# Kernel tuning notes

Measured on AMD Instinct MI355X. Metric: run time of the kernel, lower is better.

Reference implementation:

```python
import jax, jax.numpy as jnp
import numpy as np

DIM = 1024
HEADS = 16
HEAD_DIM = DIM // HEADS
SCALE = HEAD_DIM ** -0.5


def setup_inputs() -> dict:
    key = jax.random.key(0)
    k1, k2, k3 = jax.random.split(key, 3)
    x = jax.random.normal(k1, (4, 2048, DIM), dtype=jnp.float32)
    # nn.Linear weight shape [out, in]; y = x @ W.T
    W_qkv = jax.random.normal(k2, (3 * DIM, DIM), dtype=jnp.float32) * (DIM ** -0.5)
    W_proj = jax.random.normal(k3, (DIM, DIM), dtype=jnp.float32) * (DIM ** -0.5)
    b_proj = jnp.zeros((DIM,), dtype=jnp.float32)
    return {"x": x, "W_qkv": W_qkv, "W_proj": W_proj, "b_proj": b_proj}


def reference(x, W_qkv, W_proj, b_proj):
    B, N, C = x.shape
    qkv = x @ W_qkv.T  # [B, N, 3C]
    qkv = qkv.reshape(B, N, 3, HEADS, HEAD_DIM).transpose(2, 0, 3, 1, 4)  # [3,B,H,N,D]
    q, k, v = qkv[0], qkv[1], qkv[2]
    attn = jnp.einsum('bhnd,bhmd->bhnm', q, k) * SCALE
    attn = jax.nn.softmax(attn, axis=-1)
    out = jnp.einsum('bhnm,bhmd->bhnd', attn, v)  # [B,H,N,D]
    out = out.transpose(0, 2, 1, 3).reshape(B, N, C)
    return out @ W_proj.T + b_proj
```

## Files before the change

kernel.cpp:

```cpp
#include <hip/hip_runtime.h>
#include <hip/hip_bf16.h>
#include <stdint.h>

typedef __attribute__((ext_vector_type(8))) __bf16 bf16x8;
typedef __attribute__((ext_vector_type(4))) float f32x4;
typedef __attribute__((ext_vector_type(16))) float f32x16;
typedef __attribute__((ext_vector_type(8))) unsigned short u16x8;
typedef __attribute__((ext_vector_type(4))) unsigned int u32x4;

#define DIM 1024
#define SEQ 2048
#define BATCH 4
#define MROWS (BATCH*SEQ)
#define QK_SCALE 0.1803368801111204f

__device__ __forceinline__ unsigned short f2bf(float f) {
  unsigned int u = __float_as_uint(f);
  u += 0x7fff + ((u >> 16) & 1);
  return (unsigned short)(u >> 16);
}

__device__ __forceinline__ void async16(const void* g, void* l) {
  __builtin_amdgcn_global_load_lds(
      (const __attribute__((address_space(1))) unsigned int*)g,
      (__attribute__((address_space(3))) unsigned int*)l, 16, 0, 0);
}

__device__ __forceinline__ unsigned cvtpk(float lo, float hi) {
  unsigned r;
  asm("v_cvt_pk_bf16_f32 %0, %1, %2" : "=v"(r) : "v"(lo), "v"(hi));
  return r;
}

__global__ __launch_bounds__(256) void cvt3(
    const float* __restrict__ x, const float* __restrict__ w1,
    const float* __restrict__ w2, unsigned short* __restrict__ xb,
    unsigned short* __restrict__ w1b, unsigned short* __restrict__ w2b) {
  const size_t NX = (size_t)MROWS * DIM;
  const size_t NW1 = (size_t)3 * DIM * DIM;
  const size_t NW2 = (size_t)DIM * DIM;
  size_t i = ((size_t)blockIdx.x * blockDim.x + threadIdx.x) * 8;
  const float* s; unsigned short* d; size_t off;
  if (i < NX) { s = x; d = xb; off = i; }
  else if (i < NX + NW1) { s = w1; d = w1b; off = i - NX; }
  else if (i < NX + NW1 + NW2) { s = w2; d = w2b; off = i - NX - NW1; }
  else return;
  float4 a = *(const float4*)(s + off);
  float4 b = *(const float4*)(s + off + 4);
  u16x8 r;
  r[0] = f2bf(a.x); r[1] = f2bf(a.y); r[2] = f2bf(a.z); r[3] = f2bf(a.w);
  r[4] = f2bf(b.x); r[5] = f2bf(b.y); r[6] = f2bf(b.z); r[7] = f2bf(b.w);
  *(u16x8*)(d + off) = r;
}

template<int OUT_BF16>
__global__ __launch_bounds__(256) void gemm_bt(
    const unsigned short* __restrict__ A, const unsigned short* __restrict__ Bt,
    unsigned short* __restrict__ Cb, float* __restrict__ Cf,
    const float* __restrict__ bias, int M, int N, int K,
    float qscale, int qcols)
{
  __shared__ unsigned short Asm[128 * 64];
  __shared__ unsigned short Bsm[128 * 64];

  int nwg = gridDim.x;
  int bid = blockIdx.x;
  int cpx = nwg >> 3;
  int wg = (bid & 7) * cpx + (bid >> 3);
  int ntn = N >> 7;
  int tn = wg % ntn, tm = wg / ntn;

  int t = threadIdx.x, l = t & 63, w = t >> 6;
  int lr = l & 15, lg = l >> 4;
  int wr = w >> 1, wc = w & 1;

  f32x4 acc[4][4] = {};

  const unsigned short* Ab = A + (size_t)tm * 128 * K;
  const unsigned short* Bb = Bt + (size_t)tn * 128 * K;

  for (int k0 = 0; k0 < K; k0 += 64) {
    #pragma unroll
    for (int i = 0; i < 4; ++i) {
      int idx = i * 256 + t;
      int row = idx >> 3, cc = (idx & 7) * 8;
      async16(Ab + (size_t)row * K + k0 + cc, (char*)Asm + idx * 16);
      async16(Bb + (size_t)row * K + k0 + cc, (char*)Bsm + idx * 16);
    }
    __syncthreads();
    #pragma unroll
    for (int kk = 0; kk < 2; ++kk) {
      bf16x8 af[4], bfr[4];
      #pragma unroll
      for (int m = 0; m < 4; ++m)
        af[m] = *(const bf16x8*)&Asm[(wr * 64 + m * 16 + lr) * 64 + kk * 32 + lg * 8];
      #pragma unroll
      for (int n = 0; n < 4; ++n)
        bfr[n] = *(const bf16x8*)&Bsm[(wc * 64 + n * 16 + lr) * 64 + kk * 32 + lg * 8];
      #pragma unroll
      for (int m = 0; m < 4; ++m)
        #pragma unroll
        for (int n = 0; n < 4; ++n)
          acc[m][n] = __builtin_amdgcn_mfma_f32_16x16x32_bf16(af[m], bfr[n], acc[m][n], 0, 0, 0);
    }
    __syncthreads();
  }

  #pragma unroll
  for (int m = 0; m < 4; ++m)
    #pragma unroll
    for (int n = 0; n < 4; ++n) {
      int col = tn * 128 + wc * 64 + n * 16 + lr;
      float cs = (OUT_BF16 && col < qcols) ? qscale : 1.0f;
      #pragma unroll
      for (int j = 0; j < 4; ++j) {
        int row = tm * 128 + wr * 64 + m * 16 + lg * 4 + j;
        if (OUT_BF16) Cb[(size_t)row * N + col] = f2bf(acc[m][n][j] * cs);
        else          Cf[(size_t)row * N + col] = acc[m][n][j] + bias[col];
      }
    }
}

__global__ __launch_bounds__(256, 4) void attn_fwd(
    const unsigned short* __restrict__ qkv, unsigned short* __restrict__ out)
{
  __shared__ unsigned short Ksm[2][64 * 64];
  __shared__ unsigned short Vt[2][64 * 64];
  __shared__ float bcast[4][32];

  const int sb = (blockIdx.x & 7) * 128 + (blockIdx.x >> 3);
  const int bh = sb >> 4;
  const int qt = sb & 15;
  const int b = bh >> 4, h = bh & 15;
  const int t = threadIdx.x, wid = t >> 6, l = t & 63;
  const int ql = l & 31, hi = l >> 5;

  const size_t RS = 3 * DIM;
  const unsigned short* base = qkv + (size_t)b * SEQ * RS + h * 64;
  const unsigned short* kb = base + DIM;
  const unsigned short* vp = base + 2 * DIM;

  const int qrow = qt * 128 + wid * 32 + ql;
  bf16x8 qf[4];
  #pragma unroll
  for (int s = 0; s < 4; ++s)
    qf[s] = *(const bf16x8*)(base + (size_t)qrow * RS + s * 16 + hi * 8);

  f32x16 oacc[2] = {};
  float rlp = 0.f;

  #define STAGE_K(KT, BUF)                                                   \
    _Pragma("unroll")                                                        \
    for (int i_ = 0; i_ < 2; ++i_) {                                         \
      int idx_ = i_ * 256 + t;                                               \
      int row_ = idx_ >> 3, pc_ = idx_ & 7;                                  \
      async16(kb + (size_t)((KT) * 64 + row_) * RS + (pc_ ^ (row_ & 7)) * 8, \
              (char*)(BUF) + idx_ * 16);                                     \
    }

  #define LOAD_V(KT, VA, VB)                                                 \
    {                                                                        \
      const unsigned short* p_ = vp + (size_t)((KT) * 64 + (t & 63)) * RS +  \
                                 (t >> 6) * 16;                              \
      VA = *(const u16x8*)p_;                                                \
      VB = *(const u16x8*)(p_ + 8);                                          \
    }

  #define WRITE_V(BUF, VA, VB)                                               \
    {                                                                        \
      int vn_ = t & 63, dg_ = t >> 6;                                        \
      int pc_ = (vn_ & 51) | ((vn_ & 4) << 1) | ((vn_ & 8) >> 1);            \
      _Pragma("unroll")                                                      \
      for (int j_ = 0; j_ < 8; ++j_) {                                       \
        int d0_ = dg_ * 16 + j_, d1_ = d0_ + 8;                              \
        (BUF)[d0_ * 64 + (((pc_ >> 3) ^ (d0_ & 7)) << 3) + (pc_ & 7)] = (VA)[j_]; \
        (BUF)[d1_ * 64 + (((pc_ >> 3) ^ (d1_ & 7)) << 3) + (pc_ & 7)] = (VB)[j_]; \
      }                                                                      \
    }

  {
    u16x8 va, vb2;
    STAGE_K(0, Ksm[0]);
    LOAD_V(0, va, vb2);
    WRITE_V(Vt[0], va, vb2);
  }
  __syncthreads();

  const int NT = SEQ / 64;
  int cur = 0;
  for (int kt = 0; kt < NT; ++kt) {
    u16x8 va, vb2;
    const bool pf = (kt + 1 < NT);
    if (pf) {
      STAGE_K(kt + 1, Ksm[cur ^ 1]);
      LOAD_V(kt + 1, va, vb2);
    }

    f32x16 st[2];
    __builtin_amdgcn_s_setprio(1);
    #pragma unroll
    for (int ti = 0; ti < 2; ++ti) {
      f32x16 a = {};
      int row = ti * 32 + ql;
      #pragma unroll
      for (int s = 0; s < 4; ++s) {
        bf16x8 af = *(const bf16x8*)&Ksm[cur][row * 64 + (((2 * s + hi) ^ (row & 7)) << 3)];
        a = __builtin_amdgcn_mfma_f32_32x32x16_bf16(af, qf[s], a, 0, 0, 0);
      }
      st[ti] = a;
    }
    __builtin_amdgcn_s_setprio(0);

    #pragma unroll
    for (int ti = 0; ti < 2; ++ti)
      #pragma unroll
      for (int r = 0; r < 16; ++r)
        st[ti][r] = __builtin_exp2f(st[ti][r]);
    float s0[8];
    #pragma unroll
    for (int r = 0; r < 8; ++r)
      s0[r] = (st[0][r] + st[0][r + 8]) + (st[1][r] + st[1][r + 8]);
    rlp += ((s0[0] + s0[1]) + (s0[2] + s0[3])) + ((s0[4] + s0[5]) + (s0[6] + s0[7]));

    bf16x8 pa[4];
    #pragma unroll
    for (int ti = 0; ti < 2; ++ti) {
      union { u32x4 u; bf16x8 v; } c0, c1;
      #pragma unroll
      for (int j = 0; j < 4; ++j) {
        c0.u[j] = cvtpk(st[ti][2 * j],     st[ti][2 * j + 1]);
        c1.u[j] = cvtpk(st[ti][8 + 2 * j], st[ti][8 + 2 * j + 1]);
      }
      pa[2 * ti]     = c0.v;
      pa[2 * ti + 1] = c1.v;
    }

    __builtin_amdgcn_s_setprio(1);
    #pragma unroll
    for (int c = 0; c < 4; ++c) {
      #pragma unroll
      for (int dh = 0; dh < 2; ++dh) {
        int row = dh * 32 + ql;
        bf16x8 vf = *(const bf16x8*)&Vt[cur][row * 64 + (((2 * c + hi) ^ (row & 7)) << 3)];
        oacc[dh] = __builtin_amdgcn_mfma_f32_32x32x16_bf16(pa[c], vf, oacc[dh], 0, 0, 0);
      }
    }
    __builtin_amdgcn_s_setprio(0);

    if (pf) { WRITE_V(Vt[cur ^ 1], va, vb2); }
    __syncthreads();
    cur ^= 1;
  }

  {
    float rl = rlp + __shfl_xor(rlp, 32);
    float inv = 1.0f / rl;
    if (l < 32) bcast[wid][l] = inv;
    asm volatile("s_waitcnt lgkmcnt(0)" ::: "memory");
    __builtin_amdgcn_sched_barrier(0);
    f32x4 ig[4];
    #pragma unroll
    for (int g = 0; g < 4; ++g)
      ig[g] = *(const f32x4*)&bcast[wid][8 * g + 4 * hi];
    #pragma unroll
    for (int dh = 0; dh < 2; ++dh) {
      #pragma unroll
      for (int g = 0; g < 4; ++g) {
        #pragma unroll
        for (int r2 = 0; r2 < 4; ++r2) {
          int q = r2 + 8 * g + 4 * hi;
          int grow = b * SEQ + qt * 128 + wid * 32 + q;
          int gcol = h * 64 + dh * 32 + ql;
          out[(size_t)grow * DIM + gcol] = f2bf(oacc[dh][g * 4 + r2] * ig[g][r2]);
        }
      }
    }
  }
  #undef STAGE_K
  #undef LOAD_V
  #undef WRITE_V
}

extern "C" void kernel_launch(void* const* d_in, const int* in_sizes, int n_in,
                              void* d_out, int out_size, void* d_ws, size_t ws_size,
                              hipStream_t stream) {
  const float* x     = (const float*)d_in[0];
  const float* Wqkv  = (const float*)d_in[1];
  const float* Wproj = (const float*)d_in[2];
  const float* bproj = (const float*)d_in[3];
  float* out = (float*)d_out;

  unsigned short* xb    = (unsigned short*)d_ws;
  unsigned short* w1b   = xb + (size_t)MROWS * DIM;
  unsigned short* w2b   = w1b + (size_t)3 * DIM * DIM;
  unsigned short* qkvb  = w2b + (size_t)DIM * DIM;
  unsigned short* attnb = qkvb + (size_t)MROWS * 3 * DIM;

  cvt3<<<6144, 256, 0, stream>>>(x, Wqkv, Wproj, xb, w1b, w2b);
  gemm_bt<1><<<(MROWS / 128) * (3 * DIM / 128), 256, 0, stream>>>(
      xb, w1b, qkvb, nullptr, nullptr, MROWS, 3 * DIM, DIM, QK_SCALE, DIM);
  attn_fwd<<<1024, 256, 0, stream>>>(qkvb, attnb);
  gemm_bt<0><<<(MROWS / 128) * (DIM / 128), 256, 0, stream>>>(
      attnb, w2b, nullptr, out, bproj, MROWS, DIM, DIM, 1.0f, 0);
}
```

Baseline: 227.3 us.

## Use 256x256 tile GEMM for QKV projection and drop LDS broadcast in attention epilogue

Adds a new 512-thread GEMM kernel with 256x256 output tiles and double-buffered LDS (128 KB) for the QKV projection, raising data reuse per loaded tile and overlapping global loads with MFMA work. The attention epilogue replaces the shared-memory broadcast of row normalizers with wave shuffles, freeing LDS and allowing launch bounds of 5 blocks per CU. The large tile yields only 384 workgroups, which limits parallelism on a many-CU GPU, and the heavy register and LDS use caps occupancy.

```diff
diff --git a/kernel.cpp b/kernel.cpp
--- a/kernel.cpp
+++ b/kernel.cpp
@@ -53,6 +53,105 @@
   *(u16x8*)(d + off) = r;
 }
 
+__global__ __launch_bounds__(512, 2) void gemm256(
+    const unsigned short* __restrict__ A, const unsigned short* __restrict__ Bt,
+    unsigned short* __restrict__ Cb, float qscale, int qcols,
+    int M, int N, int K)
+{
+  __shared__ unsigned short Ab[2][256 * 64];
+  __shared__ unsigned short Bb[2][256 * 64];
+
+  const int nwg = gridDim.x;
+  const int cpx = nwg >> 3;
+  const int bid = blockIdx.x;
+  const int wg = (bid & 7) * cpx + (bid >> 3);
+  const int ntn = N >> 8;
+  const int tn = wg % ntn, tm = wg / ntn;
+
+  const int t = threadIdx.x, l = t & 63, w = t >> 6;
+  const int lr = l & 15, lg = l >> 4;
+  const int wr = w >> 2;
+  const int wc = w & 3;
+
+  f32x4 acc[8][4] = {};
+
+  const unsigned short* Ag = A + (size_t)(tm * 256) * K;
+  const unsigned short* Bg = Bt + (size_t)(tn * 256) * K;
+
+  int soff[4];
+  #pragma unroll
+  for (int i = 0; i < 4; ++i) {
+    int idx = i * 512 + t;
+    int row = idx >> 3, pc = idx & 7;
+    soff[i] = row * K + ((pc ^ (row & 7)) << 3);
+  }
+
+  #define STAGE(buf, kt)                                                     \
+    {                                                                        \
+      const unsigned short* a_ = Ag + (kt) * 64;                             \
+      const unsigned short* b_ = Bg + (kt) * 64;                             \
+      _Pragma("unroll")                                                      \
+      for (int i_ = 0; i_ < 4; ++i_) {                                       \
+        async16(a_ + soff[i_], (char*)Ab[buf] + (i_ * 512 + t) * 16);        \
+        async16(b_ + soff[i_], (char*)Bb[buf] + (i_ * 512 + t) * 16);        \
+      }                                                                      \
+    }
+
+  STAGE(0, 0);
+  __syncthreads();
+
+  const int NKT = K >> 6;
+  int c = 0;
+  for (int kt = 0; kt < NKT; ++kt) {
+    if (kt + 1 < NKT) STAGE(c ^ 1, kt + 1);
+    #pragma unroll
+    for (int q = 0; q < 4; ++q) {
+      const int mh = q >> 1, nh = q & 1;
+      bf16x8 af[4][2], bfr[2][2];
+      #pragma unroll
+      for (int m = 0; m < 4; ++m) {
+        int row = wr * 128 + (mh * 4 + m) * 16 + lr;
+        #pragma unroll
+        for (int kk = 0; kk < 2; ++kk)
+          af[m][kk] = *(const bf16x8*)&Ab[c][row * 64 + (((kk * 4 + lg) ^ (row & 7)) << 3)];
+      }
+      #pragma unroll
+      for (int n = 0; n < 2; ++n) {
+        int row = wc * 64 + (nh * 2 + n) * 16 + lr;
+        #pragma unroll
+        for (int kk = 0; kk < 2; ++kk)
+          bfr[n][kk] = *(const bf16x8*)&Bb[c][row * 64 + (((kk * 4 + lg) ^ (row & 7)) << 3)];
+      }
+      __builtin_amdgcn_s_setprio(1);
+      #pragma unroll
+      for (int m = 0; m < 4; ++m)
+        #pragma unroll
+        for (int n = 0; n < 2; ++n)
+          #pragma unroll
+          for (int kk = 0; kk < 2; ++kk)
+            acc[mh * 4 + m][nh * 2 + n] = __builtin_amdgcn_mfma_f32_16x16x32_bf16(
+                af[m][kk], bfr[n][kk], acc[mh * 4 + m][nh * 2 + n], 0, 0, 0);
+      __builtin_amdgcn_s_setprio(0);
+    }
+    __syncthreads();
+    c ^= 1;
+  }
+
+  #pragma unroll
+  for (int m = 0; m < 8; ++m)
+    #pragma unroll
+    for (int n = 0; n < 4; ++n) {
+      int col = tn * 256 + wc * 64 + n * 16 + lr;
+      float cs = (col < qcols) ? qscale : 1.0f;
+      #pragma unroll
+      for (int j = 0; j < 4; ++j) {
+        int row = tm * 256 + wr * 128 + m * 16 + lg * 4 + j;
+        Cb[(size_t)row * N + col] = f2bf(acc[m][n][j] * cs);
+      }
+    }
+  #undef STAGE
+}
+
 template<int OUT_BF16>
 __global__ __launch_bounds__(256) void gemm_bt(
     const unsigned short* __restrict__ A, const unsigned short* __restrict__ Bt,
@@ -121,12 +220,11 @@
     }
 }
 
-__global__ __launch_bounds__(256, 4) void attn_fwd(
+__global__ __launch_bounds__(256, 5) void attn_fwd(
     const unsigned short* __restrict__ qkv, unsigned short* __restrict__ out)
 {
   __shared__ unsigned short Ksm[2][64 * 64];
   __shared__ unsigned short Vt[2][64 * 64];
-  __shared__ float bcast[4][32];
 
   const int sb = (blockIdx.x & 7) * 128 + (blockIdx.x >> 3);
   const int bh = sb >> 4;
@@ -255,24 +353,17 @@
   {
     float rl = rlp + __shfl_xor(rlp, 32);
     float inv = 1.0f / rl;
-    if (l < 32) bcast[wid][l] = inv;
-    asm volatile("s_waitcnt lgkmcnt(0)" ::: "memory");
-    __builtin_amdgcn_sched_barrier(0);
-    f32x4 ig[4];
-    #pragma unroll
-    for (int g = 0; g < 4; ++g)
-      ig[g] = *(const f32x4*)&bcast[wid][8 * g + 4 * hi];
-    #pragma unroll
-    for (int dh = 0; dh < 2; ++dh) {
-      #pragma unroll
-      for (int g = 0; g < 4; ++g) {
-        #pragma unroll
-        for (int r2 = 0; r2 < 4; ++r2) {
-          int q = r2 + 8 * g + 4 * hi;
-          int grow = b * SEQ + qt * 128 + wid * 32 + q;
-          int gcol = h * 64 + dh * 32 + ql;
-          out[(size_t)grow * DIM + gcol] = f2bf(oacc[dh][g * 4 + r2] * ig[g][r2]);
-        }
+    const int grow0 = b * SEQ + qt * 128 + wid * 32;
+    const int gcol0 = h * 64 + ql;
+    #pragma unroll
+    for (int g = 0; g < 4; ++g) {
+      #pragma unroll
+      for (int r2 = 0; r2 < 4; ++r2) {
+        int q = r2 + 8 * g + 4 * hi;
+        float iv = __shfl(inv, q);
+        size_t rowoff = (size_t)(grow0 + q) * DIM + gcol0;
+        out[rowoff]      = f2bf(oacc[0][g * 4 + r2] * iv);
+        out[rowoff + 32] = f2bf(oacc[1][g * 4 + r2] * iv);
       }
     }
   }
@@ -297,8 +388,8 @@
   unsigned short* attnb = qkvb + (size_t)MROWS * 3 * DIM;
 
   cvt3<<<6144, 256, 0, stream>>>(x, Wqkv, Wproj, xb, w1b, w2b);
-  gemm_bt<1><<<(MROWS / 128) * (3 * DIM / 128), 256, 0, stream>>>(
-      xb, w1b, qkvb, nullptr, nullptr, MROWS, 3 * DIM, DIM, QK_SCALE, DIM);
+  gemm256<<<(MROWS / 256) * (3 * DIM / 256), 512, 0, stream>>>(
+      xb, w1b, qkvb, QK_SCALE, DIM, MROWS, 3 * DIM, DIM);
   attn_fwd<<<1024, 256, 0, stream>>>(qkvb, attnb);
   gemm_bt<0><<<(MROWS / 128) * (DIM / 128), 256, 0, stream>>>(
       attnb, w2b, nullptr, out, bproj, MROWS, DIM, DIM, 1.0f, 0);
```

Measured after the change: 429.5 us. 89.0% more time.
